# Optimization experiments

Measured on AMD Instinct MI355X. Metric: run time of the kernel, lower is better.

## Reference

```python
import jax, jax.numpy as jnp
import numpy as np

EMBED_DIM = 1024
NUM_HEADS = 16


def setup_inputs() -> dict:
    key = jax.random.key(0)
    kx, kq, kk, kv, ko = jax.random.split(key, 5)
    B, S, D = 2, 2048, EMBED_DIM
    s = 1.0 / np.sqrt(D)
    return {
        "x": jax.random.normal(kx, (B, S, D), dtype=jnp.float32),
        "Wq": jax.random.normal(kq, (D, D), dtype=jnp.float32) * s,
        "Wk": jax.random.normal(kk, (D, D), dtype=jnp.float32) * s,
        "Wv": jax.random.normal(kv, (D, D), dtype=jnp.float32) * s,
        "Wo": jax.random.normal(ko, (D, D), dtype=jnp.float32) * s,
    }


def reference(x, Wq, Wk, Wv, Wo):
    B, S, D = x.shape
    H = NUM_HEADS
    d_k = D // H
    # QKV projections (nn.Linear applies x @ W.T)
    q = (x @ Wq.T).reshape(B, S, H, d_k).transpose(0, 2, 1, 3)  # [B,H,S,d_k]
    k = (x @ Wk.T).reshape(B, S, H, d_k).transpose(0, 2, 1, 3)
    v = (x @ Wv.T).reshape(B, S, H, d_k).transpose(0, 2, 1, 3)
    scores = jnp.einsum("bhqd,bhkd->bhqk", q, k) / jnp.sqrt(jnp.float32(d_k))
    probs = jax.nn.softmax(scores, axis=-1)  # dropout is identity in eval
    attn = jnp.einsum("bhqk,bhkd->bhqd", probs, v)  # [B,H,S,d_k]
    attn = attn.transpose(0, 2, 1, 3).reshape(B, S, D)
    return attn @ Wo.T
```

## Files before the change

kernel.cpp:

```cpp
#include <hip/hip_runtime.h>
#include <stdint.h>

typedef __attribute__((ext_vector_type(4))) float    f32x4;
typedef __attribute__((ext_vector_type(8))) _Float16 half8;
typedef __attribute__((ext_vector_type(4))) _Float16 half4;
typedef unsigned long long u64;

#define MFMA16(a, b, c)    __builtin_amdgcn_mfma_f32_16x16x32_f16(a, b, c, 0, 0, 0)
#define MFMA16K16(a, b, c) __builtin_amdgcn_mfma_f32_16x16x16f16(a, b, c, 0, 0, 0)

#if __has_builtin(__builtin_amdgcn_exp2f)
#define EXP2F(x) __builtin_amdgcn_exp2f(x)
#else
#define EXP2F(x) exp2f(x)
#endif

#define CEXP 0.18033688f

__device__ inline void gl_lds16(const void* g, void* l) {
    __builtin_amdgcn_global_load_lds(
        (const __attribute__((address_space(1))) unsigned int*)g,
        (__attribute__((address_space(3))) unsigned int*)l, 16, 0, 0);
}

__global__ __launch_bounds__(256) void cast_all(
    const float* __restrict__ x,  const float* __restrict__ wq,
    const float* __restrict__ wk, const float* __restrict__ wv,
    const float* __restrict__ wo,
    _Float16* __restrict__ xh,  _Float16* __restrict__ wqh,
    _Float16* __restrict__ wkh, _Float16* __restrict__ wvh,
    _Float16* __restrict__ woh) {
    const int NX = 4194304, NW = 1048576;
    int i = (blockIdx.x * 256 + threadIdx.x) * 4;
    const float* src; _Float16* dst; int off;
    if (i < NX) { src = x; dst = xh; off = i; }
    else {
        int j = i - NX; int w = j >> 20; off = j & (NW - 1);
        src = (w == 0) ? wq : (w == 1) ? wk : (w == 2) ? wv : wo;
        dst = (w == 0) ? wqh : (w == 1) ? wkh : (w == 2) ? wvh : woh;
    }
    f32x4 v = *(const f32x4*)(src + off);
    half4 o;
    o.x = (_Float16)v.x; o.y = (_Float16)v.y; o.z = (_Float16)v.z; o.w = (_Float16)v.w;
    *(half4*)(dst + off) = o;
}

#define BN 128
#define BK 64

template <int MODE>
__global__ __launch_bounds__(256) void gemm_bt(const _Float16* __restrict__ A,
                                               const _Float16* __restrict__ B,
                                               void* __restrict__ C0,
                                               void* __restrict__ C1,
                                               void* __restrict__ C2,
                                               int M, int N, int K) {
    constexpr int BM  = (MODE == 3) ? 128 : 64;
    constexpr int MT  = BM / 32;
    constexpr int AIT = BM / 32;

    __shared__ __attribute__((aligned(16))) _Float16 smem[(BM + BN) * BK];
    _Float16* As = smem;
    _Float16* Bs = smem + BM * BK;

    const int tid  = threadIdx.x;
    const int wave = tid >> 6;
    const int lane = tid & 63;
    const int l16  = lane & 15;
    const int quad = lane >> 4;
    const int m0 = blockIdx.y * BM;
    const int n0 = blockIdx.x * BN;
    const int wm = (wave >> 1) * (BM / 2);
    const int wn = (wave & 1) * 64;

    const int srow = tid >> 3;
    const int scc  = (tid & 7) ^ ((tid >> 3) & 7);

    f32x4 acc[MT][4];
#pragma unroll
    for (int i = 0; i < MT; i++)
#pragma unroll
        for (int j = 0; j < 4; j++) acc[i][j] = (f32x4){0.f, 0.f, 0.f, 0.f};

    for (int k0 = 0; k0 < K; k0 += BK) {
        __syncthreads();
#pragma unroll
        for (int i = 0; i < AIT; i++)
            gl_lds16(A + (size_t)(m0 + i * 32 + srow) * K + k0 + scc * 8,
                     (char*)As + i * 4096 + wave * 1024);
#pragma unroll
        for (int i = 0; i < 4; i++)
            gl_lds16(B + (size_t)(n0 + i * 32 + srow) * K + k0 + scc * 8,
                     (char*)Bs + i * 4096 + wave * 1024);
        __syncthreads();

#pragma unroll
        for (int kk = 0; kk < 2; kk++) {
            half8 af[MT], bf[4];
#pragma unroll
            for (int mt = 0; mt < MT; mt++) {
                int row = wm + mt * 16 + l16;
                af[mt] = *(const half8*)(As + row * 64 + ((quad + 4 * kk) ^ (row & 7)) * 8);
            }
#pragma unroll
            for (int nt = 0; nt < 4; nt++) {
                int row = wn + nt * 16 + l16;
                bf[nt] = *(const half8*)(Bs + row * 64 + ((quad + 4 * kk) ^ (row & 7)) * 8);
            }
#pragma unroll
            for (int mt = 0; mt < MT; mt++)
#pragma unroll
                for (int nt = 0; nt < 4; nt++)
                    acc[mt][nt] = MFMA16(af[mt], bf[nt], acc[mt][nt]);
        }
    }

    if (MODE == 0) {
        float* C = (float*)C0;
#pragma unroll
        for (int mt = 0; mt < MT; mt++)
#pragma unroll
            for (int r = 0; r < 4; r++) {
                int row = m0 + wm + mt * 16 + quad * 4 + r;
                float* Crow = C + (size_t)row * N + n0 + wn + l16;
#pragma unroll
                for (int nt = 0; nt < 4; nt++) Crow[nt * 16] = acc[mt][nt][r];
            }
    } else {
        const int region = n0 >> 10;
        const int nb = (n0 & 1023) + wn;
        if (region < 2) {
            _Float16* C = (region == 0) ? (_Float16*)C0 : (_Float16*)C1;
            const float scale = (region == 0) ? CEXP : 1.f;
#pragma unroll
            for (int mt = 0; mt < MT; mt++)
#pragma unroll
                for (int r = 0; r < 4; r++) {
                    int mg = m0 + wm + mt * 16 + quad * 4 + r;
                    int b = mg >> 11, s = mg & 2047;
#pragma unroll
                    for (int nt = 0; nt < 4; nt++) {
                        int nw = nb + nt * 16 + l16;
                        int h = nw >> 6, d = nw & 63;
                        C[(((size_t)b * 16 + h) * 2048 + s) * 64 + d] =
                            (_Float16)(acc[mt][nt][r] * scale);
                    }
                }
        } else {
            __syncthreads();
            _Float16* ep = smem + wave * 4096;
#pragma unroll
            for (int mt = 0; mt < MT; mt++)
#pragma unroll
                for (int nt = 0; nt < 4; nt++) {
                    int dn = nt * 16 + l16;
                    int slot = (mt * 2 + (quad >> 1)) ^ (dn & 7);
                    union { half4 h; u64 q; } o;
#pragma unroll
                    for (int r = 0; r < 4; r++) o.h[r] = (_Float16)acc[mt][nt][r];
                    *(u64*)(ep + dn * 64 + slot * 8 + (quad & 1) * 4) = o.q;
                }
            __syncthreads();
            int mgb = m0 + wm;
            int b = mgb >> 11, sbase = mgb & 2047;
            int h = nb >> 6;
            _Float16* C = (_Float16*)C2 + ((size_t)b * 16 + h) * 64 * 2048;
#pragma unroll
            for (int j = 0; j < 8; j++) {
                int dn = j * 8 + (lane >> 3);
                int slot = (lane & 7) ^ (dn & 7);
                half8 val = *(const half8*)(ep + dn * 64 + slot * 8);
                *(half8*)(C + (size_t)dn * 2048 + sbase + (lane & 7) * 8) = val;
            }
        }
    }
}

__global__ __launch_bounds__(256) void attn_kernel(const _Float16* __restrict__ Q,
                                                   const _Float16* __restrict__ Kg,
                                                   const _Float16* __restrict__ Vt,
                                                   _Float16* __restrict__ Oa) {
    __shared__ __attribute__((aligned(16))) _Float16 Ks[64 * 64];
    __shared__ __attribute__((aligned(16))) _Float16 Vs[64 * 68];

    const int tid  = threadIdx.x;
    const int wave = tid >> 6;
    const int lane = tid & 63;
    const int l16  = lane & 15;
    const int quad = lane >> 4;
    const int bh = blockIdx.y;
    const int q0 = blockIdx.x * 128 + wave * 32;

    half8 qf[2][2];
#pragma unroll
    for (int qt = 0; qt < 2; qt++)
#pragma unroll
        for (int kk = 0; kk < 2; kk++)
            qf[qt][kk] = *(const half8*)(Q + ((size_t)bh * 2048 + q0 + qt * 16 + l16) * 64 +
                                         (quad + 4 * kk) * 8);

    const int srow = tid >> 3;
    const int sc8  = tid & 7;
    const int kslot = sc8 ^ (srow & 7);

    const _Float16* kp = Kg + (size_t)bh * 2048 * 64 + (size_t)srow * 64 + sc8 * 8;
    const _Float16* vp = Vt + (size_t)bh * 64 * 2048 + (size_t)srow * 2048 + sc8 * 8;

    f32x4 lsum4[2];
    f32x4 oacc[2][4];
#pragma unroll
    for (int qt = 0; qt < 2; qt++) {
        lsum4[qt] = (f32x4){0.f, 0.f, 0.f, 0.f};
#pragma unroll
        for (int dt = 0; dt < 4; dt++) oacc[qt][dt] = (f32x4){0.f, 0.f, 0.f, 0.f};
    }

    half8 kr0 = *(const half8*)(kp);
    half8 kr1 = *(const half8*)(kp + 32 * 64);
    half8 vr0 = *(const half8*)(vp);
    half8 vr1 = *(const half8*)(vp + 32 * 2048);

    for (int kt = 0; kt < 2048; kt += 64) {
        __syncthreads();
        *(half8*)(Ks + srow * 64 + kslot * 8) = kr0;
        *(half8*)(Ks + (srow + 32) * 64 + kslot * 8) = kr1;
        {
            union { half8 h; u64 q[2]; } u0, u1;
            u0.h = vr0; u1.h = vr1;
            _Float16* vd0 = Vs + srow * 68 + sc8 * 8;
            _Float16* vd1 = Vs + (srow + 32) * 68 + sc8 * 8;
            *(u64*)(vd0) = u0.q[0]; *(u64*)(vd0 + 4) = u0.q[1];
            *(u64*)(vd1) = u1.q[0]; *(u64*)(vd1 + 4) = u1.q[1];
        }
        __syncthreads();

        {
            int kt2 = (kt + 64) & 2047;
            kr0 = *(const half8*)(kp + (size_t)kt2 * 64);
            kr1 = *(const half8*)(kp + (size_t)(kt2 + 32) * 64);
            vr0 = *(const half8*)(vp + kt2);
            vr1 = *(const half8*)(vp + 32 * 2048 + kt2);
        }

        f32x4 sc4[2][4];
#pragma unroll
        for (int nt = 0; nt < 4; nt++) {
            int row = nt * 16 + l16;
            half8 kf0 = *(const half8*)(Ks + row * 64 + (quad ^ (row & 7)) * 8);
            half8 kf1 = *(const half8*)(Ks + row * 64 + ((quad + 4) ^ (row & 7)) * 8);
#pragma unroll
            for (int qt = 0; qt < 2; qt++) {
                f32x4 s = (f32x4){0.f, 0.f, 0.f, 0.f};
                s = MFMA16(kf0, qf[qt][0], s);
                s = MFMA16(kf1, qf[qt][1], s);
                sc4[qt][nt] = s;
            }
        }

        half4 ph[2][4];
#pragma unroll
        for (int qt = 0; qt < 2; qt++)
#pragma unroll
            for (int nt = 0; nt < 4; nt++) {
                half4 p;
#pragma unroll
                for (int r = 0; r < 4; r++) {
                    float pe = EXP2F(sc4[qt][nt][r]);
                    lsum4[qt][r] += pe;
                    p[r] = (_Float16)pe;
                }
                ph[qt][nt] = p;
            }

#pragma unroll
        for (int nt = 0; nt < 4; nt++) {
#pragma unroll
            for (int dt = 0; dt < 4; dt++) {
                int row = dt * 16 + l16;
                half4 vf = *(const half4*)(Vs + row * 68 + nt * 16 + quad * 4);
#pragma unroll
                for (int qt = 0; qt < 2; qt++)
                    oacc[qt][dt] = MFMA16K16(vf, ph[qt][nt], oacc[qt][dt]);
            }
        }
    }

    const int b = bh >> 4, h = bh & 15;
#pragma unroll
    for (int qt = 0; qt < 2; qt++) {
        float ls = (lsum4[qt][0] + lsum4[qt][1]) + (lsum4[qt][2] + lsum4[qt][3]);
        ls += __shfl_xor(ls, 16);
        ls += __shfl_xor(ls, 32);
        float inv = 1.f / ls;
        int q = q0 + qt * 16 + l16;
        _Float16* orow = Oa + ((size_t)b * 2048 + q) * 1024 + h * 64;
#pragma unroll
        for (int dt = 0; dt < 4; dt++) {
            half4 o;
#pragma unroll
            for (int r = 0; r < 4; r++) o[r] = (_Float16)(oacc[qt][dt][r] * inv);
            *(half4*)(orow + dt * 16 + quad * 4) = o;
        }
    }
}

extern "C" void kernel_launch(void* const* d_in, const int* in_sizes, int n_in,
                              void* d_out, int out_size, void* d_ws, size_t ws_size,
                              hipStream_t stream) {
    const float* x  = (const float*)d_in[0];
    const float* Wq = (const float*)d_in[1];
    const float* Wk = (const float*)d_in[2];
    const float* Wv = (const float*)d_in[3];
    const float* Wo = (const float*)d_in[4];
    float* out = (float*)d_out;

    const int NX = 2 * 2048 * 1024;
    const int NW = 1024 * 1024;

    _Float16* ws  = (_Float16*)d_ws;
    _Float16* xh  = ws;
    _Float16* wqh = xh + NX;
    _Float16* wkh = wqh + NW;
    _Float16* wvh = wkh + NW;
    _Float16* woh = wvh + NW;
    _Float16* Qb  = woh + NW;
    _Float16* Kb  = Qb + NX;
    _Float16* Vtb = Kb + NX;
    _Float16* Ab  = Vtb + NX;

    cast_all<<<8192, 256, 0, stream>>>(x, Wq, Wk, Wv, Wo, xh, wqh, wkh, wvh, woh);

    gemm_bt<3><<<dim3(3072 / 128, 4096 / 128), 256, 0, stream>>>(
        xh, wqh, Qb, Kb, Vtb, 4096, 3072, 1024);

    attn_kernel<<<dim3(16, 32), 256, 0, stream>>>(Qb, Kb, Vtb, Ab);

    gemm_bt<0><<<dim3(1024 / 128, 4096 / 64), 256, 0, stream>>>(
        Ab, woh, out, nullptr, nullptr, 4096, 1024, 1024);
}
```

Baseline: 185.7 us.

## Split attention KV range across two wave groups with LDS reduction

The attention block grows from 256 to 512 threads. Two groups of four waves each handle half of every 128-key step, using separate K/V LDS tiles, and their partial outputs and row sums are combined through shared memory at the end. The V tile moves from a padded layout to an XOR-swizzled one, which removes the split 8-byte stores. The aim is more waves per CU and half as many loop iterations per wave, at the cost of a final LDS reduction and a larger shared-memory footprint.

Result: no change. 183.1 us (-1.4%).

```diff
diff --git a/kernel.cpp b/kernel.cpp
--- a/kernel.cpp
+++ b/kernel.cpp
@@ -176,20 +176,24 @@
     }
 }
 
-__global__ __launch_bounds__(256) void attn_kernel(const _Float16* __restrict__ Q,
-                                                   const _Float16* __restrict__ Kg,
-                                                   const _Float16* __restrict__ Vt,
-                                                   _Float16* __restrict__ Oa) {
-    __shared__ __attribute__((aligned(16))) _Float16 Ks[64 * 64];
-    __shared__ __attribute__((aligned(16))) _Float16 Vs[64 * 68];
+__global__ __launch_bounds__(512, 4) void attn_kernel(const _Float16* __restrict__ Q,
+                                                      const _Float16* __restrict__ Kg,
+                                                      const _Float16* __restrict__ Vt,
+                                                      _Float16* __restrict__ Oa) {
+    __shared__ __attribute__((aligned(16))) _Float16 smem[20480];
 
     const int tid  = threadIdx.x;
     const int wave = tid >> 6;
     const int lane = tid & 63;
     const int l16  = lane & 15;
     const int quad = lane >> 4;
+    const int qw   = wave & 3;
+    const int kg   = wave >> 2;
     const int bh = blockIdx.y;
-    const int q0 = blockIdx.x * 128 + wave * 32;
+    const int q0 = blockIdx.x * 128 + qw * 32;
+
+    _Float16* Ksw = smem + kg * 4096;
+    _Float16* Vsw = smem + 8192 + kg * 4096;
 
     half8 qf[2][2];
 #pragma unroll
@@ -216,38 +220,32 @@
     }
 
     half8 kr0 = *(const half8*)(kp);
-    half8 kr1 = *(const half8*)(kp + 32 * 64);
+    half8 kr1 = *(const half8*)(kp + 64 * 64);
     half8 vr0 = *(const half8*)(vp);
-    half8 vr1 = *(const half8*)(vp + 32 * 2048);
-
-    for (int kt = 0; kt < 2048; kt += 64) {
+    half8 vr1 = *(const half8*)(vp + 64);
+
+    for (int it = 0; it < 16; it++) {
         __syncthreads();
-        *(half8*)(Ks + srow * 64 + kslot * 8) = kr0;
-        *(half8*)(Ks + (srow + 32) * 64 + kslot * 8) = kr1;
+        *(half8*)(smem + srow * 64 + kslot * 8) = kr0;
+        *(half8*)(smem + 4096 + srow * 64 + kslot * 8) = kr1;
+        *(half8*)(smem + 8192 + srow * 64 + kslot * 8) = vr0;
+        *(half8*)(smem + 12288 + srow * 64 + kslot * 8) = vr1;
+        __syncthreads();
+
         {
-            union { half8 h; u64 q[2]; } u0, u1;
-            u0.h = vr0; u1.h = vr1;
-            _Float16* vd0 = Vs + srow * 68 + sc8 * 8;
-            _Float16* vd1 = Vs + (srow + 32) * 68 + sc8 * 8;
-            *(u64*)(vd0) = u0.q[0]; *(u64*)(vd0 + 4) = u0.q[1];
-            *(u64*)(vd1) = u1.q[0]; *(u64*)(vd1 + 4) = u1.q[1];
-        }
-        __syncthreads();
-
-        {
-            int kt2 = (kt + 64) & 2047;
-            kr0 = *(const half8*)(kp + (size_t)kt2 * 64);
-            kr1 = *(const half8*)(kp + (size_t)(kt2 + 32) * 64);
-            vr0 = *(const half8*)(vp + kt2);
-            vr1 = *(const half8*)(vp + 32 * 2048 + kt2);
+            int ktp2 = ((it + 1) & 15) * 128;
+            kr0 = *(const half8*)(kp + (size_t)ktp2 * 64);
+            kr1 = *(const half8*)(kp + (size_t)(ktp2 + 64) * 64);
+            vr0 = *(const half8*)(vp + ktp2);
+            vr1 = *(const half8*)(vp + ktp2 + 64);
         }
 
         f32x4 sc4[2][4];
 #pragma unroll
         for (int nt = 0; nt < 4; nt++) {
             int row = nt * 16 + l16;
-            half8 kf0 = *(const half8*)(Ks + row * 64 + (quad ^ (row & 7)) * 8);
-            half8 kf1 = *(const half8*)(Ks + row * 64 + ((quad + 4) ^ (row & 7)) * 8);
+            half8 kf0 = *(const half8*)(Ksw + row * 64 + (quad ^ (row & 7)) * 8);
+            half8 kf1 = *(const half8*)(Ksw + row * 64 + ((quad + 4) ^ (row & 7)) * 8);
 #pragma unroll
             for (int qt = 0; qt < 2; qt++) {
                 f32x4 s = (f32x4){0.f, 0.f, 0.f, 0.f};
@@ -277,7 +275,8 @@
 #pragma unroll
             for (int dt = 0; dt < 4; dt++) {
                 int row = dt * 16 + l16;
-                half4 vf = *(const half4*)(Vs + row * 68 + nt * 16 + quad * 4);
+                int ch  = (nt * 2 + (quad >> 1)) ^ (row & 7);
+                half4 vf = *(const half4*)(Vsw + row * 64 + ch * 8 + (quad & 1) * 4);
 #pragma unroll
                 for (int qt = 0; qt < 2; qt++)
                     oacc[qt][dt] = MFMA16K16(vf, ph[qt][nt], oacc[qt][dt]);
@@ -285,21 +284,43 @@
         }
     }
 
-    const int b = bh >> 4, h = bh & 15;
-#pragma unroll
-    for (int qt = 0; qt < 2; qt++) {
-        float ls = (lsum4[qt][0] + lsum4[qt][1]) + (lsum4[qt][2] + lsum4[qt][3]);
-        ls += __shfl_xor(ls, 16);
-        ls += __shfl_xor(ls, 32);
-        float inv = 1.f / ls;
-        int q = q0 + qt * 16 + l16;
-        _Float16* orow = Oa + ((size_t)b * 2048 + q) * 1024 + h * 64;
-#pragma unroll
-        for (int dt = 0; dt < 4; dt++) {
-            half4 o;
-#pragma unroll
-            for (int r = 0; r < 4; r++) o[r] = (_Float16)(oacc[qt][dt][r] * inv);
-            *(half4*)(orow + dt * 16 + quad * 4) = o;
+    __syncthreads();
+    float* rp = (float*)smem + qw * 2560;
+    if (kg == 1) {
+#pragma unroll
+        for (int qt = 0; qt < 2; qt++)
+#pragma unroll
+            for (int dt = 0; dt < 4; dt++)
+                *(f32x4*)(rp + ((qt * 4 + dt) * 64 + lane) * 4) = oacc[qt][dt];
+        *(f32x4*)(rp + (8 * 64 + lane) * 4) = lsum4[0];
+        *(f32x4*)(rp + (9 * 64 + lane) * 4) = lsum4[1];
+    }
+    __syncthreads();
+    if (kg == 0) {
+#pragma unroll
+        for (int qt = 0; qt < 2; qt++)
+#pragma unroll
+            for (int dt = 0; dt < 4; dt++)
+                oacc[qt][dt] += *(const f32x4*)(rp + ((qt * 4 + dt) * 64 + lane) * 4);
+        lsum4[0] += *(const f32x4*)(rp + (8 * 64 + lane) * 4);
+        lsum4[1] += *(const f32x4*)(rp + (9 * 64 + lane) * 4);
+
+        const int b = bh >> 4, h = bh & 15;
+#pragma unroll
+        for (int qt = 0; qt < 2; qt++) {
+            float ls = (lsum4[qt][0] + lsum4[qt][1]) + (lsum4[qt][2] + lsum4[qt][3]);
+            ls += __shfl_xor(ls, 16);
+            ls += __shfl_xor(ls, 32);
+            float inv = 1.f / ls;
+            int q = q0 + qt * 16 + l16;
+            _Float16* orow = Oa + ((size_t)b * 2048 + q) * 1024 + h * 64;
+#pragma unroll
+            for (int dt = 0; dt < 4; dt++) {
+                half4 o;
+#pragma unroll
+                for (int r = 0; r < 4; r++) o[r] = (_Float16)(oacc[qt][dt][r] * inv);
+                *(half4*)(orow + dt * 16 + quad * 4) = o;
+            }
         }
     }
 }
@@ -333,7 +354,7 @@
     gemm_bt<3><<<dim3(3072 / 128, 4096 / 128), 256, 0, stream>>>(
         xh, wqh, Qb, Kb, Vtb, 4096, 3072, 1024);
 
-    attn_kernel<<<dim3(16, 32), 256, 0, stream>>>(Qb, Kb, Vtb, Ab);
+    attn_kernel<<<dim3(16, 32), 512, 0, stream>>>(Qb, Kb, Vtb, Ab);
 
     gemm_bt<0><<<dim3(1024 / 128, 4096 / 64), 256, 0, stream>>>(
         Ab, woh, out, nullptr, nullptr, 4096, 1024, 1024);
```
